# Kernel tuning notes

Hardware: AMD Instinct MI355X
Metric: run time of the kernel (lower is better)

## Reference

```python
import jax, jax.numpy as jnp
import numpy as np

B, T, D, E, P, DA = 4, 2048, 1024, 6, 36, 512
THRESHOLD = 0.3
LN_EPS = 1e-5
# pair (i, j) index tables: full 6x6 directed graph, row-major like the torch loop
PI = jnp.asarray(np.repeat(np.arange(E), E))  # (36,) source expert
PJ = jnp.asarray(np.tile(np.arange(E), E))    # (36,) target expert


def setup_inputs() -> dict:
    key = jax.random.key(0)
    ks = jax.random.split(key, 16)
    def n(k, shape, scale=0.02):
        return jax.random.normal(k, shape, dtype=jnp.float32) * scale
    return {
        "bridge_output": jax.random.normal(ks[0], (B, T, D), dtype=jnp.float32),
        "expert_outputs": jax.random.normal(ks[1], (E, B, T, D), dtype=jnp.float32),
        "expert_weights": jax.random.uniform(ks[2], (B, T, E), dtype=jnp.float32),
        "cond_query": n(ks[3], (E, D)),
        "cond_Wk": n(ks[4], (E, D, D)), "cond_bk": jnp.zeros((E, D), jnp.float32),
        "cond_Wv": n(ks[5], (E, D, D)), "cond_bv": jnp.zeros((E, D), jnp.float32),
        "pair_Wa": n(ks[6], (P, D, DA)), "pair_ba": jnp.zeros((P, DA), jnp.float32),
        "pair_Wb": n(ks[7], (P, D, DA)), "pair_bb": jnp.zeros((P, DA), jnp.float32),
        "gate_W1": n(ks[8], (P, 2 * DA, DA)), "gate_b1": jnp.zeros((P, DA), jnp.float32),
        "gate_W2": n(ks[9], (P, DA, 1)), "gate_b2": jnp.zeros((P, 1), jnp.float32),
        "syn_W1": n(ks[10], (P, 2 * DA, D)), "syn_b1": jnp.zeros((P, D), jnp.float32),
        "syn_W2": n(ks[11], (P, D, D)), "syn_b2": jnp.zeros((P, D), jnp.float32),
        "pair_gate": jnp.full((P,), 0.01, jnp.float32),
        "ln_gamma": jnp.ones((D,), jnp.float32), "ln_beta": jnp.zeros((D,), jnp.float32),
        "out_W": n(ks[12], (D, D)), "out_b": jnp.zeros((D,), jnp.float32),
        "analogy_gate": jnp.asarray(0.05, jnp.float32),
    }


def reference(bridge_output, expert_outputs, expert_weights,
              cond_query, cond_Wk, cond_bk, cond_Wv, cond_bv,
              pair_Wa, pair_ba, pair_Wb, pair_bb,
              gate_W1, gate_b1, gate_W2, gate_b2,
              syn_W1, syn_b1, syn_W2, syn_b2, pair_gate,
              ln_gamma, ln_beta, out_W, out_b, analogy_gate):
    scale = D ** -0.5
    # --- ProverbCondenser, batched over E experts ---
    w = jnp.moveaxis(expert_weights, -1, 0)[..., None]          # (E,B,T,1)
    x = expert_outputs * w                                       # (E,B,T,D)
    k = jnp.einsum('ebtd,edf->ebtf', x, cond_Wk) + cond_bk[:, None, None, :]
    v = jnp.einsum('ebtd,edf->ebtf', x, cond_Wv) + cond_bv[:, None, None, :]
    logits = jnp.einsum('ef,ebtf->ebt', cond_query, k) * scale   # (E,B,T)
    attn = jax.nn.softmax(logits, axis=-1)
    formulas = jnp.einsum('ebt,ebtf->ebf', attn, v)              # (E,B,D)
    # --- 36 AnalogyPairs, batched over leading P axis ---
    fa = formulas[PI]                                            # (P,B,D)
    fb = formulas[PJ]                                            # (P,B,D)
    a = jnp.einsum('pbd,pda->pba', fa, pair_Wa) + pair_ba[:, None, :]
    b = jnp.einsum('pbd,pda->pba', fb, pair_Wb) + pair_bb[:, None, :]
    c = jnp.concatenate([a, b], axis=-1)                         # (P,B,2*DA)
    h = jax.nn.gelu(jnp.einsum('pbc,pca->pba', c, gate_W1) + gate_b1[:, None, :], approximate=False)
    strength = jax.nn.sigmoid(jnp.einsum('pba,pao->pbo', h, gate_W2) + gate_b2[:, None, :])  # (P,B,1)
    hs = jax.nn.gelu(jnp.einsum('pbc,pcd->pbd', c, syn_W1) + syn_b1[:, None, :], approximate=False)
    insight = (jnp.einsum('pbd,pde->pbe', hs, syn_W2) + syn_b2[:, None, :]) * pair_gate[:, None, None]  # (P,B,D)
    # --- threshold-masked weighted combine (replaces the .item() branch) ---
    avg_strength = jnp.mean(strength, axis=(1, 2))               # (P,)
    mask = (avg_strength > THRESHOLD).astype(insight.dtype)      # (P,)
    active_count = jnp.sum(mask)
    total = jnp.einsum('p,pbd->bd', mask, insight * strength)    # (B,D)
    total = total / jnp.maximum(active_count, 1.0)
    # output_proj: LayerNorm + Linear
    mu = jnp.mean(total, axis=-1, keepdims=True)
    var = jnp.mean((total - mu) ** 2, axis=-1, keepdims=True)
    normed = (total - mu) / jnp.sqrt(var + LN_EPS) * ln_gamma + ln_beta
    projected = normed @ out_W + out_b                           # (B,D)
    addition = projected[:, None, :] * analogy_gate              # (B,1,D) broadcast over T
    output = jnp.where(active_count > 0, bridge_output + addition, bridge_output)
    return output, avg_strength, active_count
```

## Files before the change

### kernel.cpp

```cpp
#include <hip/hip_runtime.h>
#include <math.h>

#define cB 4
#define cT 2048
#define cD 1024
#define cE 6
#define cP 36
#define cDA 512
#define SCALE 0.03125f
#define LN_EPS 1e-5f
#define THRESH 0.3f

#define OFF_QK      0
#define OFF_COEFF   6144
#define OFF_XBAR    55296
#define OFF_FORM    79872
#define OFF_C       104448
#define OFF_H       251904
#define OFF_HS      325632
#define OFF_INS     473088
#define OFF_STR     620544
#define OFF_MASK    620688
#define OFF_CNT     620724
#define OFF_NORMED  620728
#define OFF_ADD     624824

__device__ __forceinline__ float gelu_f(float x){
  return 0.5f * x * (1.f + erff(x * 0.70710678118654752440f));
}

__global__ void k_init(float* __restrict__ ws,
                       const float* __restrict__ bv, const float* __restrict__ ba,
                       const float* __restrict__ bb, const float* __restrict__ b1,
                       const float* __restrict__ bs1, const float* __restrict__ bs2,
                       const float* __restrict__ outb){
  int i = blockIdx.x * 256 + threadIdx.x;
  if (i < 24576){ ws[OFF_XBAR + i] = 0.f; return; }
  i -= 24576;
  if (i < 24576){ int f = i & 1023; int e = i >> 12; ws[OFF_FORM + i] = bv[e*cD + f]; return; }
  i -= 24576;
  if (i < 147456){ int j = i & 1023; int p = i >> 12;
    ws[OFF_C + i] = (j < cDA) ? ba[p*cDA + j] : bb[p*cDA + j - cDA]; return; }
  i -= 147456;
  if (i < 73728){ int j = i & 511; int p = i >> 11; ws[OFF_H + i] = b1[p*cDA + j]; return; }
  i -= 73728;
  if (i < 147456){ int j = i & 1023; int p = i >> 12; ws[OFF_HS + i] = bs1[p*cD + j]; return; }
  i -= 147456;
  if (i < 147456){ int j = i & 1023; int p = i >> 12; ws[OFF_INS + i] = bs2[p*cD + j]; return; }
  i -= 147456;
  if (i < 4096){ ws[OFF_ADD + i] = outb[i & 1023]; return; }
}

__global__ void k_qk(const float* __restrict__ Wk, const float* __restrict__ q,
                     float* __restrict__ qk){
  int wid = (blockIdx.x * 256 + threadIdx.x) >> 6;
  int lane = threadIdx.x & 63;
  if (wid >= cE * cD) return;
  int e = wid >> 10;
  const float4* wrow = (const float4*)(Wk + (size_t)wid * cD);
  const float4* qrow = (const float4*)(q + e * cD);
  float acc = 0.f;
  #pragma unroll
  for (int it = 0; it < 4; ++it){
    float4 w4 = wrow[it*64 + lane];
    float4 q4 = qrow[it*64 + lane];
    acc += w4.x*q4.x + w4.y*q4.y + w4.z*q4.z + w4.w*q4.w;
  }
  for (int off = 32; off; off >>= 1) acc += __shfl_down(acc, off);
  if (lane == 0) qk[wid] = acc;
}

__global__ void k_logits(const float* __restrict__ eo, const float* __restrict__ ew,
                         const float* __restrict__ qk, float* __restrict__ coeff){
  int wid = (blockIdx.x * 256 + threadIdx.x) >> 6;
  int lane = threadIdx.x & 63;
  int e = wid / (cB * cT);
  int bt = wid % (cB * cT);
  const float4* row = (const float4*)(eo + (size_t)wid * cD);
  const float4* q4p = (const float4*)(qk + e * cD);
  float acc = 0.f;
  #pragma unroll
  for (int it = 0; it < 4; ++it){
    float4 a = row[it*64 + lane];
    float4 b = q4p[it*64 + lane];
    acc += a.x*b.x + a.y*b.y + a.z*b.z + a.w*b.w;
  }
  for (int off = 32; off; off >>= 1) acc += __shfl_down(acc, off);
  if (lane == 0){
    int b = bt / cT, t = bt % cT;
    coeff[wid] = acc * ew[(b*cT + t)*cE + e] * SCALE;
  }
}

__global__ void k_softmax(float* __restrict__ coeff, const float* __restrict__ ew){
  int eb = blockIdx.x; int e = eb / cB, b = eb % cB;
  float* row = coeff + (size_t)eb * cT;
  __shared__ float red[256];
  int tid = threadIdx.x;
  float v[8]; float m = -INFINITY;
  #pragma unroll
  for (int k = 0; k < 8; ++k){ v[k] = row[tid + k*256]; m = fmaxf(m, v[k]); }
  red[tid] = m; __syncthreads();
  for (int s = 128; s; s >>= 1){ if (tid < s) red[tid] = fmaxf(red[tid], red[tid+s]); __syncthreads(); }
  m = red[0]; __syncthreads();
  float sum = 0.f;
  #pragma unroll
  for (int k = 0; k < 8; ++k){ v[k] = expf(v[k] - m); sum += v[k]; }
  red[tid] = sum; __syncthreads();
  for (int s = 128; s; s >>= 1){ if (tid < s) red[tid] += red[tid+s]; __syncthreads(); }
  float inv = 1.f / red[0];
  #pragma unroll
  for (int k = 0; k < 8; ++k){
    int t = tid + k*256;
    row[t] = v[k] * inv * ew[(b*cT + t)*cE + e];
  }
}

__global__ void k_xbar(const float* __restrict__ eo, const float* __restrict__ coeff,
                       float* __restrict__ xbar){
  int bid = blockIdx.x;
  int seg = bid & 7;  bid >>= 3;
  int dch = bid & 3;  bid >>= 2;
  int b   = bid & 3;  bid >>= 2;
  int e   = bid;
  int tid = threadIdx.x;
  int eb = e * cB + b;
  __shared__ float sc[256];
  sc[tid] = coeff[(size_t)eb*cT + seg*256 + tid];
  __syncthreads();
  const float* base = eo + ((size_t)eb*cT + seg*256)*cD + dch*256 + tid;
  float acc = 0.f;
  #pragma unroll 4
  for (int tt = 0; tt < 256; ++tt) acc += sc[tt] * base[(size_t)tt * cD];
  atomicAdd(&xbar[eb*cD + dch*256 + tid], acc);
}

__global__ void k_formulas(const float* __restrict__ Wv, const float* __restrict__ xbar,
                           float* __restrict__ form){
  int bid = blockIdx.x;
  int dch = bid & 7; bid >>= 3;
  int fch = bid & 3; bid >>= 2;
  int e = bid;
  int tid = threadIdx.x;
  __shared__ float4 xl[128];
  if (tid < 128){
    float4 v;
    v.x = xbar[(e*cB+0)*cD + dch*128 + tid];
    v.y = xbar[(e*cB+1)*cD + dch*128 + tid];
    v.z = xbar[(e*cB+2)*cD + dch*128 + tid];
    v.w = xbar[(e*cB+3)*cD + dch*128 + tid];
    xl[tid] = v;
  }
  __syncthreads();
  float a0=0,a1=0,a2=0,a3=0;
  const float* wbase = Wv + (size_t)e*cD*cD + (size_t)(dch*128)*cD + fch*256 + tid;
  #pragma unroll 8
  for (int dd = 0; dd < 128; ++dd){
    float w = wbase[(size_t)dd * cD];
    float4 x = xl[dd];
    a0 += x.x*w; a1 += x.y*w; a2 += x.z*w; a3 += x.w*w;
  }
  int o = fch*256 + tid;
  atomicAdd(&form[(e*cB+0)*cD + o], a0);
  atomicAdd(&form[(e*cB+1)*cD + o], a1);
  atomicAdd(&form[(e*cB+2)*cD + o], a2);
  atomicAdd(&form[(e*cB+3)*cD + o], a3);
}

__global__ void k_gemv(const float* __restrict__ in, const float* __restrict__ W,
                       float* __restrict__ out, const float* __restrict__ form,
                       int Din, int Dout, int nC, int outStride, int colOff,
                       int gatherMode, int actGelu){
  int nD = Din >> 8;
  int bid = blockIdx.x;
  int dch = bid % nD; bid /= nD;
  int cch = bid % nC; bid /= nC;
  int p = bid;
  int tid = threadIdx.x;
  __shared__ float4 il[256];
  const float* inbase;
  if (gatherMode){
    int e = (gatherMode == 1) ? (p / cE) : (p % cE);
    inbase = form + (size_t)e * cB * cD;
  } else {
    inbase = in + (size_t)p * cB * Din;
  }
  int d0 = dch << 8;
  {
    float4 v;
    v.x = inbase[0*Din + d0 + tid];
    v.y = inbase[1*Din + d0 + tid];
    v.z = inbase[2*Din + d0 + tid];
    v.w = inbase[3*Din + d0 + tid];
    if (actGelu){ v.x = gelu_f(v.x); v.y = gelu_f(v.y); v.z = gelu_f(v.z); v.w = gelu_f(v.w); }
    il[tid] = v;
  }
  __syncthreads();
  float a0=0,a1=0,a2=0,a3=0;
  const float* wbase = W + (size_t)p*Din*Dout + (size_t)d0*Dout + (cch<<8) + tid;
  #pragma unroll 8
  for (int dd = 0; dd < 256; ++dd){
    float w = wbase[(size_t)dd * Dout];
    float4 x = il[dd];
    a0 += x.x*w; a1 += x.y*w; a2 += x.z*w; a3 += x.w*w;
  }
  size_t ob = (size_t)p*cB*outStride + colOff + (cch<<8) + tid;
  atomicAdd(&out[ob],                 a0);
  atomicAdd(&out[ob +   outStride],   a1);
  atomicAdd(&out[ob + 2*outStride],   a2);
  atomicAdd(&out[ob + 3*outStride],   a3);
}

__global__ void k_strength(const float* __restrict__ pre_h, const float* __restrict__ W2,
                           const float* __restrict__ b2, float* __restrict__ str){
  int p = blockIdx.x;
  int b = threadIdx.x >> 6;
  int lane = threadIdx.x & 63;
  const float* h = pre_h + (size_t)(p*cB + b)*cDA;
  const float* w = W2 + (size_t)p*cDA;
  float acc = 0.f;
  #pragma unroll
  for (int it = 0; it < 8; ++it){
    int j = it*64 + lane;
    acc += gelu_f(h[j]) * w[j];
  }
  for (int off = 32; off; off >>= 1) acc += __shfl_down(acc, off);
  if (lane == 0) str[p*cB + b] = 1.f / (1.f + expf(-(acc + b2[p])));
}

__global__ void k_combine(const float* __restrict__ str, float* __restrict__ ws,
                          float* __restrict__ out_tail){
  int tid = threadIdx.x;
  __shared__ float mk[64];
  float msk = 0.f;
  if (tid < cP){
    float avg = 0.25f * (str[tid*4] + str[tid*4+1] + str[tid*4+2] + str[tid*4+3]);
    out_tail[tid] = avg;
    msk = (avg > THRESH) ? 1.f : 0.f;
    ws[OFF_MASK + tid] = msk;
  }
  mk[tid] = msk;
  __syncthreads();
  if (tid == 0){
    float cnt = 0.f;
    for (int i = 0; i < cP; ++i) cnt += mk[i];
    out_tail[cP] = cnt;
    ws[OFF_CNT]     = (cnt > 0.f) ? 1.f : 0.f;
    ws[OFF_CNT + 1] = 1.f / fmaxf(cnt, 1.f);
  }
}

__global__ void k_totln(const float* __restrict__ ins, const float* __restrict__ str,
                        const float* __restrict__ mask, const float* __restrict__ pg,
                        const float* __restrict__ cnt2, const float* __restrict__ gamma,
                        const float* __restrict__ beta, float* __restrict__ normed){
  int b = blockIdx.x;
  int tid = threadIdx.x;
  __shared__ float sc[cP];
  __shared__ float red[256];
  if (tid < cP) sc[tid] = mask[tid] * str[tid*4 + b] * pg[tid] * cnt2[1];
  __syncthreads();
  float tot[4];
  #pragma unroll
  for (int k = 0; k < 4; ++k){
    int d = tid + k*256;
    float s = 0.f;
    for (int p = 0; p < cP; ++p) s += sc[p] * ins[(size_t)(p*cB + b)*cD + d];
    tot[k] = s;
  }
  float lsum = tot[0] + tot[1] + tot[2] + tot[3];
  red[tid] = lsum; __syncthreads();
  for (int s = 128; s; s >>= 1){ if (tid < s) red[tid] += red[tid+s]; __syncthreads(); }
  float mu = red[0] * (1.f / cD); __syncthreads();
  float q = 0.f;
  #pragma unroll
  for (int k = 0; k < 4; ++k){ float dxy = tot[k] - mu; q += dxy*dxy; }
  red[tid] = q; __syncthreads();
  for (int s = 128; s; s >>= 1){ if (tid < s) red[tid] += red[tid+s]; __syncthreads(); }
  float rs = rsqrtf(red[0] * (1.f / cD) + LN_EPS);
  #pragma unroll
  for (int k = 0; k < 4; ++k){
    int d = tid + k*256;
    normed[b*cD + d] = (tot[k] - mu) * rs * gamma[d] + beta[d];
  }
}

__global__ void k_proj(const float* __restrict__ normed, const float* __restrict__ W,
                       float* __restrict__ addp){
  int bid = blockIdx.x;
  int dch = bid & 7; int fch = bid >> 3;
  int tid = threadIdx.x;
  __shared__ float4 nl[128];
  if (tid < 128){
    float4 v;
    v.x = normed[0*cD + dch*128 + tid];
    v.y = normed[1*cD + dch*128 + tid];
    v.z = normed[2*cD + dch*128 + tid];
    v.w = normed[3*cD + dch*128 + tid];
    nl[tid] = v;
  }
  __syncthreads();
  float a0=0,a1=0,a2=0,a3=0;
  const float* wbase = W + (size_t)(dch*128)*cD + fch*256 + tid;
  #pragma unroll 8
  for (int dd = 0; dd < 128; ++dd){
    float w = wbase[(size_t)dd * cD];
    float4 x = nl[dd];
    a0 += x.x*w; a1 += x.y*w; a2 += x.z*w; a3 += x.w*w;
  }
  int o = fch*256 + tid;
  atomicAdd(&addp[0*cD + o], a0);
  atomicAdd(&addp[1*cD + o], a1);
  atomicAdd(&addp[2*cD + o], a2);
  atomicAdd(&addp[3*cD + o], a3);
}

__global__ void k_final(const float* __restrict__ bridge, const float* __restrict__ addp,
                        const float* __restrict__ cnt2, const float* __restrict__ gate,
                        float* __restrict__ out){
  float g = gate[0] * cnt2[0];
  const float4* b4 = (const float4*)bridge;
  const float4* a4 = (const float4*)addp;
  float4* o4 = (float4*)out;
  int total4 = cB*cT*cD/4;
  for (int i = blockIdx.x*256 + threadIdx.x; i < total4; i += gridDim.x*256){
    float4 bb = b4[i];
    int b = i >> 19;
    float4 aa = a4[b*256 + (i & 255)];
    bb.x += g*aa.x; bb.y += g*aa.y; bb.z += g*aa.z; bb.w += g*aa.w;
    o4[i] = bb;
  }
}

extern "C" void kernel_launch(void* const* d_in, const int* in_sizes, int n_in,
                              void* d_out, int out_size, void* d_ws, size_t ws_size,
                              hipStream_t stream) {
  const float* bridge = (const float*)d_in[0];
  const float* eo     = (const float*)d_in[1];
  const float* ew     = (const float*)d_in[2];
  const float* q      = (const float*)d_in[3];
  const float* Wk     = (const float*)d_in[4];
  const float* Wv     = (const float*)d_in[6];
  const float* bv     = (const float*)d_in[7];
  const float* Wa     = (const float*)d_in[8];
  const float* ba     = (const float*)d_in[9];
  const float* Wb     = (const float*)d_in[10];
  const float* bb     = (const float*)d_in[11];
  const float* W1     = (const float*)d_in[12];
  const float* b1     = (const float*)d_in[13];
  const float* W2     = (const float*)d_in[14];
  const float* b2     = (const float*)d_in[15];
  const float* Ws1    = (const float*)d_in[16];
  const float* bs1    = (const float*)d_in[17];
  const float* Ws2    = (const float*)d_in[18];
  const float* bs2    = (const float*)d_in[19];
  const float* pg     = (const float*)d_in[20];
  const float* gamma  = (const float*)d_in[21];
  const float* beta   = (const float*)d_in[22];
  const float* outW   = (const float*)d_in[23];
  const float* outb   = (const float*)d_in[24];
  const float* agate  = (const float*)d_in[25];
  float* out = (float*)d_out;
  float* ws  = (float*)d_ws;

  k_init<<<2224, 256, 0, stream>>>(ws, bv, ba, bb, b1, bs1, bs2, outb);
  k_qk<<<1536, 256, 0, stream>>>(Wk, q, ws + OFF_QK);
  k_logits<<<12288, 256, 0, stream>>>(eo, ew, ws + OFF_QK, ws + OFF_COEFF);
  k_softmax<<<24, 256, 0, stream>>>(ws + OFF_COEFF, ew);
  k_xbar<<<768, 256, 0, stream>>>(eo, ws + OFF_COEFF, ws + OFF_XBAR);
  k_formulas<<<192, 256, 0, stream>>>(Wv, ws + OFF_XBAR, ws + OFF_FORM);
  k_gemv<<<288, 256, 0, stream>>>(nullptr, Wa, ws + OFF_C, ws + OFF_FORM,
                                  1024, 512, 2, 1024, 0,   1, 0);
  k_gemv<<<288, 256, 0, stream>>>(nullptr, Wb, ws + OFF_C, ws + OFF_FORM,
                                  1024, 512, 2, 1024, 512, 2, 0);
  k_gemv<<<288, 256, 0, stream>>>(ws + OFF_C, W1, ws + OFF_H, nullptr,
                                  1024, 512, 2, 512, 0, 0, 0);
  k_gemv<<<576, 256, 0, stream>>>(ws + OFF_C, Ws1, ws + OFF_HS, nullptr,
                                  1024, 1024, 4, 1024, 0, 0, 0);
  k_strength<<<36, 256, 0, stream>>>(ws + OFF_H, W2, b2, ws + OFF_STR);
  k_gemv<<<576, 256, 0, stream>>>(ws + OFF_HS, Ws2, ws + OFF_INS, nullptr,
                                  1024, 1024, 4, 1024, 0, 0, 1);
  k_combine<<<1, 64, 0, stream>>>(ws + OFF_STR, ws, out + (size_t)cB*cT*cD);
  k_totln<<<4, 256, 0, stream>>>(ws + OFF_INS, ws + OFF_STR, ws + OFF_MASK, pg,
                                 ws + OFF_CNT, gamma, beta, ws + OFF_NORMED);
  k_proj<<<32, 256, 0, stream>>>(ws + OFF_NORMED, outW, ws + OFF_ADD);
  k_final<<<2048, 256, 0, stream>>>(bridge, ws + OFF_ADD, ws + OFF_CNT, agate, out);
}
```

Baseline: 792.9 us.

## Fuse logits, softmax and weighted sum into one online-softmax pass; vectorize gemv

Replaces the logits, softmax and xbar kernels with a single flash-style online-softmax kernel. Each wave reads 16 expert-output rows once, computing the dot product and the running weighted sum together, and a merge kernel then combines the 128 partials per (e,b). This avoids reading the 200MB expert_outputs tensor twice. The gemv kernel now uses float4 weight loads, a 128-row d-chunk split across 4 wave groups, and a shared-memory reduction. The cost is a roughly 12MB partial-sum buffer plus an extra merge pass.

```diff
diff --git a/kernel.cpp b/kernel.cpp
--- a/kernel.cpp
+++ b/kernel.cpp
@@ -10,20 +10,23 @@
 #define SCALE 0.03125f
 #define LN_EPS 1e-5f
 #define THRESH 0.3f
+#define NW 128
+#define ROWS 16
 
 #define OFF_QK      0
-#define OFF_COEFF   6144
-#define OFF_XBAR    55296
-#define OFF_FORM    79872
-#define OFF_C       104448
-#define OFF_H       251904
-#define OFF_HS      325632
-#define OFF_INS     473088
-#define OFF_STR     620544
-#define OFF_MASK    620688
-#define OFF_CNT     620724
-#define OFF_NORMED  620728
-#define OFF_ADD     624824
+#define OFF_XBAR    6144
+#define OFF_FORM    30720
+#define OFF_C       55296
+#define OFF_H       202752
+#define OFF_HS      276480
+#define OFF_INS     423936
+#define OFF_STR     571392
+#define OFF_MASK    571536
+#define OFF_CNT     571572
+#define OFF_NORMED  571576
+#define OFF_ADD     575672
+#define OFF_APART   579768
+#define OFF_MS      3725496
 
 __device__ __forceinline__ float gelu_f(float x){
   return 0.5f * x * (1.f + erff(x * 0.70710678118654752440f));
@@ -35,8 +38,6 @@
                        const float* __restrict__ bs1, const float* __restrict__ bs2,
                        const float* __restrict__ outb){
   int i = blockIdx.x * 256 + threadIdx.x;
-  if (i < 24576){ ws[OFF_XBAR + i] = 0.f; return; }
-  i -= 24576;
   if (i < 24576){ int f = i & 1023; int e = i >> 12; ws[OFF_FORM + i] = bv[e*cD + f]; return; }
   i -= 24576;
   if (i < 147456){ int j = i & 1023; int p = i >> 12;
@@ -70,69 +71,78 @@
   if (lane == 0) qk[wid] = acc;
 }
 
-__global__ void k_logits(const float* __restrict__ eo, const float* __restrict__ ew,
-                         const float* __restrict__ qk, float* __restrict__ coeff){
-  int wid = (blockIdx.x * 256 + threadIdx.x) >> 6;
+__global__ void k_fused(const float* __restrict__ eo, const float* __restrict__ ew,
+                        const float* __restrict__ qk, float* __restrict__ Apart,
+                        float* __restrict__ ms){
+  int gw = (blockIdx.x * 256 + threadIdx.x) >> 6;
   int lane = threadIdx.x & 63;
-  int e = wid / (cB * cT);
-  int bt = wid % (cB * cT);
-  const float4* row = (const float4*)(eo + (size_t)wid * cD);
-  const float4* q4p = (const float4*)(qk + e * cD);
+  int eb = gw >> 7;
+  int seg = gw & (NW - 1);
+  int e = eb >> 2, b = eb & 3;
+  const float4* q4 = (const float4*)(qk + e * cD);
+  float4 qv0 = q4[lane], qv1 = q4[64 + lane], qv2 = q4[128 + lane], qv3 = q4[192 + lane];
+  float4 A0 = {0,0,0,0}, A1 = {0,0,0,0}, A2 = {0,0,0,0}, A3 = {0,0,0,0};
+  float m = -INFINITY, s = 0.f;
+  size_t rowbase = (size_t)eb * cT + seg * ROWS;
+  const float* ewb = ew + ((size_t)b * cT + seg * ROWS) * cE + e;
+  for (int r = 0; r < ROWS; ++r){
+    const float4* row = (const float4*)(eo + (rowbase + r) * cD);
+    float4 x0 = row[lane], x1 = row[64 + lane], x2 = row[128 + lane], x3 = row[192 + lane];
+    float dot = x0.x*qv0.x + x0.y*qv0.y + x0.z*qv0.z + x0.w*qv0.w
+              + x1.x*qv1.x + x1.y*qv1.y + x1.z*qv1.z + x1.w*qv1.w
+              + x2.x*qv2.x + x2.y*qv2.y + x2.z*qv2.z + x2.w*qv2.w
+              + x3.x*qv3.x + x3.y*qv3.y + x3.z*qv3.z + x3.w*qv3.w;
+    #pragma unroll
+    for (int off = 1; off < 64; off <<= 1) dot += __shfl_xor(dot, off);
+    float ewv = ewb[r * cE];
+    float l = dot * ewv * SCALE;
+    float mnew = fmaxf(m, l);
+    float corr = __expf(m - mnew);
+    float f = __expf(l - mnew);
+    s = s * corr + f;
+    float g = f * ewv;
+    A0.x = A0.x*corr + g*x0.x; A0.y = A0.y*corr + g*x0.y; A0.z = A0.z*corr + g*x0.z; A0.w = A0.w*corr + g*x0.w;
+    A1.x = A1.x*corr + g*x1.x; A1.y = A1.y*corr + g*x1.y; A1.z = A1.z*corr + g*x1.z; A1.w = A1.w*corr + g*x1.w;
+    A2.x = A2.x*corr + g*x2.x; A2.y = A2.y*corr + g*x2.y; A2.z = A2.z*corr + g*x2.z; A2.w = A2.w*corr + g*x2.w;
+    A3.x = A3.x*corr + g*x3.x; A3.y = A3.y*corr + g*x3.y; A3.z = A3.z*corr + g*x3.z; A3.w = A3.w*corr + g*x3.w;
+    m = mnew;
+  }
+  float4* Ap = (float4*)(Apart + (size_t)gw * cD);
+  Ap[lane] = A0; Ap[64 + lane] = A1; Ap[128 + lane] = A2; Ap[192 + lane] = A3;
+  if (lane == 0){ ms[gw*2] = m; ms[gw*2 + 1] = s; }
+}
+
+__global__ void k_merge(const float* __restrict__ Apart, const float* __restrict__ ms,
+                        float* __restrict__ xbar){
+  int bid = blockIdx.x;
+  int dch = bid & 15; int eb = bid >> 4;
+  int tid = threadIdx.x;
+  __shared__ float wgt[NW];
+  __shared__ float red[NW];
+  if (tid < NW) red[tid] = ms[(eb*NW + tid)*2];
+  __syncthreads();
+  for (int s = 64; s; s >>= 1){ if (tid < s) red[tid] = fmaxf(red[tid], red[tid+s]); __syncthreads(); }
+  float M = red[0]; __syncthreads();
+  if (tid < NW){
+    float mi = ms[(eb*NW + tid)*2], si = ms[(eb*NW + tid)*2 + 1];
+    float f = __expf(mi - M);
+    wgt[tid] = f;
+    red[tid] = si * f;
+  }
+  __syncthreads();
+  for (int s = 64; s; s >>= 1){ if (tid < s) red[tid] += red[tid+s]; __syncthreads(); }
+  float invS = 1.f / red[0];
+  __syncthreads();
+  int d = dch*64 + (tid & 63);
+  int ig = tid >> 6;
   float acc = 0.f;
-  #pragma unroll
-  for (int it = 0; it < 4; ++it){
-    float4 a = row[it*64 + lane];
-    float4 b = q4p[it*64 + lane];
-    acc += a.x*b.x + a.y*b.y + a.z*b.z + a.w*b.w;
-  }
-  for (int off = 32; off; off >>= 1) acc += __shfl_down(acc, off);
-  if (lane == 0){
-    int b = bt / cT, t = bt % cT;
-    coeff[wid] = acc * ew[(b*cT + t)*cE + e] * SCALE;
-  }
-}
-
-__global__ void k_softmax(float* __restrict__ coeff, const float* __restrict__ ew){
-  int eb = blockIdx.x; int e = eb / cB, b = eb % cB;
-  float* row = coeff + (size_t)eb * cT;
-  __shared__ float red[256];
-  int tid = threadIdx.x;
-  float v[8]; float m = -INFINITY;
-  #pragma unroll
-  for (int k = 0; k < 8; ++k){ v[k] = row[tid + k*256]; m = fmaxf(m, v[k]); }
-  red[tid] = m; __syncthreads();
-  for (int s = 128; s; s >>= 1){ if (tid < s) red[tid] = fmaxf(red[tid], red[tid+s]); __syncthreads(); }
-  m = red[0]; __syncthreads();
-  float sum = 0.f;
-  #pragma unroll
-  for (int k = 0; k < 8; ++k){ v[k] = expf(v[k] - m); sum += v[k]; }
-  red[tid] = sum; __syncthreads();
-  for (int s = 128; s; s >>= 1){ if (tid < s) red[tid] += red[tid+s]; __syncthreads(); }
-  float inv = 1.f / red[0];
-  #pragma unroll
-  for (int k = 0; k < 8; ++k){
-    int t = tid + k*256;
-    row[t] = v[k] * inv * ew[(b*cT + t)*cE + e];
-  }
-}
-
-__global__ void k_xbar(const float* __restrict__ eo, const float* __restrict__ coeff,
-                       float* __restrict__ xbar){
-  int bid = blockIdx.x;
-  int seg = bid & 7;  bid >>= 3;
-  int dch = bid & 3;  bid >>= 2;
-  int b   = bid & 3;  bid >>= 2;
-  int e   = bid;
-  int tid = threadIdx.x;
-  int eb = e * cB + b;
-  __shared__ float sc[256];
-  sc[tid] = coeff[(size_t)eb*cT + seg*256 + tid];
-  __syncthreads();
-  const float* base = eo + ((size_t)eb*cT + seg*256)*cD + dch*256 + tid;
-  float acc = 0.f;
-  #pragma unroll 4
-  for (int tt = 0; tt < 256; ++tt) acc += sc[tt] * base[(size_t)tt * cD];
-  atomicAdd(&xbar[eb*cD + dch*256 + tid], acc);
+  for (int i = ig; i < NW; i += 4)
+    acc += Apart[((size_t)(eb*NW + i))*cD + d] * wgt[i];
+  __shared__ float r2[4][64];
+  r2[ig][tid & 63] = acc;
+  __syncthreads();
+  if (ig == 0)
+    xbar[eb*cD + d] = (r2[0][tid&63] + r2[1][tid&63] + r2[2][tid&63] + r2[3][tid&63]) * invS;
 }
 
 __global__ void k_formulas(const float* __restrict__ Wv, const float* __restrict__ xbar,
@@ -169,15 +179,19 @@
 
 __global__ void k_gemv(const float* __restrict__ in, const float* __restrict__ W,
                        float* __restrict__ out, const float* __restrict__ form,
-                       int Din, int Dout, int nC, int outStride, int colOff,
+                       int Din, int Dout, int colOff, int outStride,
                        int gatherMode, int actGelu){
-  int nD = Din >> 8;
+  int nD = Din >> 7;
+  int nC = Dout >> 8;
   int bid = blockIdx.x;
   int dch = bid % nD; bid /= nD;
   int cch = bid % nC; bid /= nC;
   int p = bid;
   int tid = threadIdx.x;
-  __shared__ float4 il[256];
+  int c4 = tid & 63;
+  int dr = tid >> 6;
+  int d0 = dch << 7;
+  __shared__ float4 xl[128];
   const float* inbase;
   if (gatherMode){
     int e = (gatherMode == 1) ? (p / cE) : (p % cE);
@@ -185,30 +199,38 @@
   } else {
     inbase = in + (size_t)p * cB * Din;
   }
-  int d0 = dch << 8;
-  {
+  if (tid < 128){
     float4 v;
     v.x = inbase[0*Din + d0 + tid];
     v.y = inbase[1*Din + d0 + tid];
     v.z = inbase[2*Din + d0 + tid];
     v.w = inbase[3*Din + d0 + tid];
     if (actGelu){ v.x = gelu_f(v.x); v.y = gelu_f(v.y); v.z = gelu_f(v.z); v.w = gelu_f(v.w); }
-    il[tid] = v;
-  }
-  __syncthreads();
-  float a0=0,a1=0,a2=0,a3=0;
-  const float* wbase = W + (size_t)p*Din*Dout + (size_t)d0*Dout + (cch<<8) + tid;
-  #pragma unroll 8
-  for (int dd = 0; dd < 256; ++dd){
-    float w = wbase[(size_t)dd * Dout];
-    float4 x = il[dd];
-    a0 += x.x*w; a1 += x.y*w; a2 += x.z*w; a3 += x.w*w;
-  }
-  size_t ob = (size_t)p*cB*outStride + colOff + (cch<<8) + tid;
-  atomicAdd(&out[ob],                 a0);
-  atomicAdd(&out[ob +   outStride],   a1);
-  atomicAdd(&out[ob + 2*outStride],   a2);
-  atomicAdd(&out[ob + 3*outStride],   a3);
+    xl[tid] = v;
+  }
+  __syncthreads();
+  float4 a0 = {0,0,0,0}, a1 = {0,0,0,0}, a2 = {0,0,0,0}, a3 = {0,0,0,0};
+  const float4* wbase = (const float4*)(W + (size_t)p*Din*Dout + (size_t)d0*Dout + (cch<<8)) + c4;
+  int wstride = Dout >> 2;
+  for (int dd = dr; dd < 128; dd += 4){
+    float4 w4 = wbase[(size_t)dd * wstride];
+    float4 x = xl[dd];
+    a0.x += x.x*w4.x; a0.y += x.x*w4.y; a0.z += x.x*w4.z; a0.w += x.x*w4.w;
+    a1.x += x.y*w4.x; a1.y += x.y*w4.y; a1.z += x.y*w4.z; a1.w += x.y*w4.w;
+    a2.x += x.z*w4.x; a2.y += x.z*w4.y; a2.z += x.z*w4.z; a2.w += x.z*w4.w;
+    a3.x += x.w*w4.x; a3.y += x.w*w4.y; a3.z += x.w*w4.z; a3.w += x.w*w4.w;
+  }
+  __shared__ float4 red[4][64][4];
+  red[dr][c4][0] = a0; red[dr][c4][1] = a1; red[dr][c4][2] = a2; red[dr][c4][3] = a3;
+  __syncthreads();
+  float4 r;
+  float4 t0 = red[0][c4][dr], t1 = red[1][c4][dr], t2 = red[2][c4][dr], t3 = red[3][c4][dr];
+  r.x = t0.x + t1.x + t2.x + t3.x;
+  r.y = t0.y + t1.y + t2.y + t3.y;
+  r.z = t0.z + t1.z + t2.z + t3.z;
+  r.w = t0.w + t1.w + t2.w + t3.w;
+  float* op = out + (size_t)p*cB*outStride + (size_t)dr*outStride + colOff + (cch<<8) + c4*4;
+  atomicAdd(op+0, r.x); atomicAdd(op+1, r.y); atomicAdd(op+2, r.z); atomicAdd(op+3, r.w);
 }
 
 __global__ void k_strength(const float* __restrict__ pre_h, const float* __restrict__ W2,
@@ -363,23 +385,22 @@
   float* out = (float*)d_out;
   float* ws  = (float*)d_ws;
 
-  k_init<<<2224, 256, 0, stream>>>(ws, bv, ba, bb, b1, bs1, bs2, outb);
+  k_init<<<2128, 256, 0, stream>>>(ws, bv, ba, bb, b1, bs1, bs2, outb);
   k_qk<<<1536, 256, 0, stream>>>(Wk, q, ws + OFF_QK);
-  k_logits<<<12288, 256, 0, stream>>>(eo, ew, ws + OFF_QK, ws + OFF_COEFF);
-  k_softmax<<<24, 256, 0, stream>>>(ws + OFF_COEFF, ew);
-  k_xbar<<<768, 256, 0, stream>>>(eo, ws + OFF_COEFF, ws + OFF_XBAR);
+  k_fused<<<768, 256, 0, stream>>>(eo, ew, ws + OFF_QK, ws + OFF_APART, ws + OFF_MS);
+  k_merge<<<384, 256, 0, stream>>>(ws + OFF_APART, ws + OFF_MS, ws + OFF_XBAR);
   k_formulas<<<192, 256, 0, stream>>>(Wv, ws + OFF_XBAR, ws + OFF_FORM);
-  k_gemv<<<288, 256, 0, stream>>>(nullptr, Wa, ws + OFF_C, ws + OFF_FORM,
-                                  1024, 512, 2, 1024, 0,   1, 0);
-  k_gemv<<<288, 256, 0, stream>>>(nullptr, Wb, ws + OFF_C, ws + OFF_FORM,
-                                  1024, 512, 2, 1024, 512, 2, 0);
-  k_gemv<<<288, 256, 0, stream>>>(ws + OFF_C, W1, ws + OFF_H, nullptr,
-                                  1024, 512, 2, 512, 0, 0, 0);
-  k_gemv<<<576, 256, 0, stream>>>(ws + OFF_C, Ws1, ws + OFF_HS, nullptr,
-                                  1024, 1024, 4, 1024, 0, 0, 0);
+  k_gemv<<<576, 256, 0, stream>>>(nullptr, Wa, ws + OFF_C, ws + OFF_FORM,
+                                  1024, 512, 0, 1024, 1, 0);
+  k_gemv<<<576, 256, 0, stream>>>(nullptr, Wb, ws + OFF_C, ws + OFF_FORM,
+                                  1024, 512, 512, 1024, 2, 0);
+  k_gemv<<<576, 256, 0, stream>>>(ws + OFF_C, W1, ws + OFF_H, nullptr,
+                                  1024, 512, 0, 512, 0, 0);
+  k_gemv<<<1152, 256, 0, stream>>>(ws + OFF_C, Ws1, ws + OFF_HS, nullptr,
+                                   1024, 1024, 0, 1024, 0, 0);
   k_strength<<<36, 256, 0, stream>>>(ws + OFF_H, W2, b2, ws + OFF_STR);
-  k_gemv<<<576, 256, 0, stream>>>(ws + OFF_HS, Ws2, ws + OFF_INS, nullptr,
-                                  1024, 1024, 4, 1024, 0, 0, 1);
+  k_gemv<<<1152, 256, 0, stream>>>(ws + OFF_HS, Ws2, ws + OFF_INS, nullptr,
+                                   1024, 1024, 0, 1024, 0, 1);
   k_combine<<<1, 64, 0, stream>>>(ws + OFF_STR, ws, out + (size_t)cB*cT*cD);
   k_totln<<<4, 256, 0, stream>>>(ws + OFF_INS, ws + OFF_STR, ws + OFF_MASK, pg,
                                  ws + OFF_CNT, gamma, beta, ws + OFF_NORMED);
```

Measured after the change: 809.2 us. 2.1% more time.
